# Optimization experiments

Measured on AMD Instinct MI355X. Metric: run time of the kernel, lower is better.

The kernel has to match this reference:

```python
import jax, jax.numpy as jnp
import numpy as np

ALPHA = 0.2        # LeakyReLU negative slope
MASK_VAL = -9e15   # matches torch zero_vec constant
B, N, F, H, D = 32, 1024, 64, 3, 16  # batch, nodes, in_features, heads, head_dim


def setup_inputs() -> dict:
    key = jax.random.key(0)
    k1, k2, k3 = jax.random.split(key, 3)
    h = jax.random.normal(k1, (B, N, F), dtype=jnp.float32)
    adj = jnp.ones((N, N), dtype=jnp.float32)  # fully-connected graph ('full')
    W = jax.random.normal(k2, (H, F, D), dtype=jnp.float32) * 0.15  # ~xavier gain 1.414
    a = jax.random.normal(k3, (H, 2 * D, 1), dtype=jnp.float32) * 0.25
    return {"h": h, "adj": adj, "W": W, "a": a}


def reference(h, adj, W, a):
    # Multi-head GAT, vectorized over heads (original loops over heads).
    d = W.shape[-1]
    Wh = jnp.einsum('bnf,hfd->bhnd', h, W)              # (B,H,N,D)
    a1 = a[:, :d, 0]                                    # (H,D) -> applies to source node i
    a2 = a[:, d:, 0]                                    # (H,D) -> applies to target node j
    s1 = jnp.einsum('bhnd,hd->bhn', Wh, a1)             # (B,H,N)
    s2 = jnp.einsum('bhnd,hd->bhn', Wh, a2)             # (B,H,N)
    # e[b,h,i,j] = LeakyReLU(a1.Wh_i + a2.Wh_j) -- equivalent to the repeat/concat trick
    e = jax.nn.leaky_relu(s1[..., :, None] + s2[..., None, :], ALPHA)  # (B,H,N,N)
    e = jnp.where(adj > 0, e, MASK_VAL)
    attn = jax.nn.softmax(e, axis=-1)                   # softmax over neighbors j
    out = jnp.einsum('bhij,bhjd->bhid', attn, Wh)       # (B,H,N,D)
    # concat heads along feature dim: (B,N,H*D)
    Bn, Nn = h.shape[0], h.shape[1]
    return out.transpose(0, 2, 1, 3).reshape(Bn, Nn, -1)
```

## Files before the change

kernel.cpp:

```cpp
#include <hip/hip_runtime.h>
#include <math.h>

constexpr int Bc = 32, Nn = 1024, Fc = 64, Hc = 3, Dc = 16;
constexpr float ALPHAc = 0.2f;
constexpr float L2E    = 1.44269504088896340736f;

__device__ __forceinline__ unsigned enc_f32(float x) {
    unsigned b = __builtin_bit_cast(unsigned, x);
    return (b & 0x80000000u) ? ~b : (b | 0x80000000u);
}
__device__ __forceinline__ float dec_f32(unsigned e) {
    unsigned b = (e & 0x80000000u) ? (e ^ 0x80000000u) : ~e;
    return __builtin_bit_cast(float, b);
}

template <int CTRL, int RMASK, bool BC>
__device__ __forceinline__ float dpp_acc(float x) {
    int s = __builtin_amdgcn_update_dpp(0, __builtin_bit_cast(int, x),
                                        CTRL, RMASK, 0xF, BC);
    return x + __builtin_bit_cast(float, s);
}
__device__ __forceinline__ float wave_incl_scan(float x) {
    x = dpp_acc<0x111, 0xF, true >(x);
    x = dpp_acc<0x112, 0xF, true >(x);
    x = dpp_acc<0x114, 0xF, true >(x);
    x = dpp_acc<0x118, 0xF, true >(x);
    x = dpp_acc<0x142, 0xa, false>(x);
    x = dpp_acc<0x143, 0xc, false>(x);
    return x;
}

__device__ __forceinline__ unsigned lane_xor(unsigned x, int s) {
    if (s == 1)
        return (unsigned)__builtin_amdgcn_update_dpp(0, (int)x, 0xB1, 0xF, 0xF, true);
    if (s == 2)
        return (unsigned)__builtin_amdgcn_update_dpp(0, (int)x, 0x4E, 0xF, 0xF, true);
    return (unsigned)__shfl_xor((int)x, s, 64);
}

__global__ __launch_bounds__(1024, 1) void gat_one(
    const float* __restrict__ hbuf, const float* __restrict__ W,
    const float* __restrict__ a, const float* __restrict__ adj,
    unsigned* __restrict__ rowful, float* Whf, float* __restrict__ out)
{
    __shared__ __align__(16) float    PS[1025 * 35];
    __shared__ __align__(16) unsigned skA[Nn], skB[Nn];
    __shared__ __align__(16) float    s2o[Nn];
    __shared__ float    wtot[16][34];
    __shared__ unsigned wmiss[16];

    int bh = blockIdx.x;
    int hh = bh % Hc, b = bh / Hc;
    int t  = threadIdx.x;
    int wv = t >> 6, lane = t & 63;

    int row0 = bh * 11;
    unsigned miss = 0;
#pragma unroll
    for (int rr = 0; rr < 11; ++rr) {
        int row = row0 + rr;
        if (row < Nn) {
            float av = adj[(size_t)row * Nn + t];
            miss |= (av > 0.f) ? 0u : (1u << rr);
        }
    }
#pragma unroll
    for (int off = 1; off < 64; off <<= 1)
        miss |= (unsigned)__shfl_xor((int)miss, off, 64);
    if (lane == 0) wmiss[wv] = miss;
    __syncthreads();
    if (t < 11) {
        int row = row0 + t;
        if (row < Nn) {
            unsigned m = 0;
#pragma unroll
            for (int w2 = 0; w2 < 16; ++w2) m |= wmiss[w2];
            unsigned full = ((m >> t) & 1u) ^ 1u;
            unsigned val  = 0x5AFE0000u | ((unsigned)row << 1) | full;
            __hip_atomic_store(&rowful[row], val, __ATOMIC_RELAXED,
                               __HIP_MEMORY_SCOPE_AGENT);
        }
    }

    const float4* h4 = (const float4*)(hbuf + ((size_t)b * Nn + t) * Fc);
    const float*  Wp = W + (size_t)hh * Fc * Dc;

    float acc[Dc];
#pragma unroll
    for (int d = 0; d < Dc; ++d) acc[d] = 0.f;

#pragma unroll
    for (int q = 0; q < Fc / 4; ++q) {
        float4 hv = h4[q];
#pragma unroll
        for (int c = 0; c < 4; ++c) {
            float hv1 = (c == 0) ? hv.x : (c == 1) ? hv.y : (c == 2) ? hv.z : hv.w;
            const float4* wrp = (const float4*)(Wp + (4 * q + c) * Dc);
#pragma unroll
            for (int u = 0; u < 4; ++u) {
                float4 wq = wrp[u];
                acc[4*u+0] = fmaf(hv1, wq.x, acc[4*u+0]);
                acc[4*u+1] = fmaf(hv1, wq.y, acc[4*u+1]);
                acc[4*u+2] = fmaf(hv1, wq.z, acc[4*u+2]);
                acc[4*u+3] = fmaf(hv1, wq.w, acc[4*u+3]);
            }
        }
    }

    float4* wf = (float4*)(Whf + ((size_t)bh * Nn + t) * Dc);
#pragma unroll
    for (int u = 0; u < 4; ++u)
        wf[u] = make_float4(acc[4*u+0], acc[4*u+1], acc[4*u+2], acc[4*u+3]);

    const float* ap = a + (size_t)hh * 2 * Dc;
    float s1v = 0.f, s2v = 0.f;
#pragma unroll
    for (int d = 0; d < Dc; ++d) {
        s1v = fmaf(acc[d], ap[d],      s1v);
        s2v = fmaf(acc[d], ap[Dc + d], s2v);
    }
    s2o[t] = s2v;

    unsigned key = (enc_f32(s2v) & ~1023u) | (unsigned)t;

#pragma unroll
    for (int k = 2; k <= 64; k <<= 1) {
#pragma unroll
        for (int s = k >> 1; s >= 1; s >>= 1) {
            unsigned other = lane_xor(key, s);
            bool dirUp = ((t & k) == 0);
            bool lower = ((lane & s) == 0);
            unsigned mn = key < other ? key : other;
            unsigned mx = key < other ? other : key;
            key = (lower == dirUp) ? mn : mx;
        }
    }
    unsigned* bufs[2] = {skA, skB};
    int pb = 0;
#pragma unroll
    for (int k = 128; k <= 1024; k <<= 1) {
#pragma unroll
        for (int s = k >> 1; s >= 64; s >>= 1) {
            bufs[pb][t] = key;
            __syncthreads();
            unsigned other = bufs[pb][t ^ s];
            bool dirUp = ((t & k) == 0);
            bool lower = ((t & s) == 0);
            unsigned mn = key < other ? key : other;
            unsigned mx = key < other ? other : key;
            key = (lower == dirUp) ? mn : mx;
            pb ^= 1;
        }
#pragma unroll
        for (int s = 32; s >= 1; s >>= 1) {
            unsigned other = lane_xor(key, s);
            bool dirUp = ((t & k) == 0);
            bool lower = ((lane & s) == 0);
            unsigned mn = key < other ? key : other;
            unsigned mx = key < other ? other : key;
            key = (lower == dirUp) ? mn : mx;
        }
    }
    unsigned* sorted = bufs[pb];
    sorted[t] = key;

    int   j  = key & 1023u;
    float sv = dec_f32((key & ~1023u) | 512u);
    float Bv = __builtin_amdgcn_exp2f(sv * L2E);
    float Dv = __builtin_amdgcn_exp2f(sv * (ALPHAc * L2E));
    const float4* wr = (const float4*)(Whf + ((size_t)bh * Nn + j) * Dc);
    float4 w0 = wr[0], w1 = wr[1], w2 = wr[2], w3 = wr[3];
    float wh[16] = {w0.x,w0.y,w0.z,w0.w, w1.x,w1.y,w1.z,w1.w,
                    w2.x,w2.y,w2.z,w2.w, w3.x,w3.y,w3.z,w3.w};

    float v[34];
#pragma unroll
    for (int d = 0; d < 16; ++d) {
        v[d]      = Bv * wh[d];
        v[16 + d] = Dv * wh[d];
    }
    v[32] = Bv; v[33] = Dv;

#pragma unroll
    for (int c = 0; c < 34; ++c) {
        float inc = wave_incl_scan(v[c]);
        if (lane == 63) wtot[wv][c] = inc;
        v[c] = inc - v[c];
    }
    __syncthreads();

    if (t < 544) {
        int c = t >> 4, w = t & 15;
        float own = wtot[w][c];
        float x = own;
#pragma unroll
        for (int off = 1; off < 16; off <<= 1) {
            float o = __shfl_up(x, off, 16);
            if ((lane & 15) >= off) x += o;
        }
        wtot[w][c] = x - own;
        if (w == 15) PS[(size_t)1024 * 35 + c] = x;
    }
    __syncthreads();

    float* myrow = PS + (size_t)t * 35;
#pragma unroll
    for (int c = 0; c < 34; ++c)
        myrow[c] = v[c] + wtot[wv][c];
    __syncthreads();

    int i = t;
    float R  = __builtin_amdgcn_exp2f(-0.8f * L2E * s1v);
    float* op = out + ((size_t)b * Nn + i) * (Hc * Dc) + hh * Dc;

    unsigned expv = 0x5AFE0000u | ((unsigned)i << 1) | 1u;
    unsigned fv;
    do {
        fv = __hip_atomic_load(&rowful[i], __ATOMIC_RELAXED,
                               __HIP_MEMORY_SCOPE_AGENT);
    } while ((fv | 1u) != expv);

    if (fv & 1u) {
        unsigned qk = (enc_f32(-s1v) & ~1023u) | 1023u;
        int p = 0;
#pragma unroll
        for (int step = 512; step >= 1; step >>= 1)
            if (sorted[p + step - 1] <= qk) p += step;

        const float* Pp = PS + (size_t)p * 35;
        const float* Tp = PS + (size_t)1024 * 35;
        float den = (Tp[32] - Pp[32]) + R * Pp[33];
        float inv = 1.0f / den;
#pragma unroll
        for (int u = 0; u < 4; ++u) {
            float o0 = ((Tp[4*u+0] - Pp[4*u+0]) + R * Pp[16 + 4*u+0]) * inv;
            float o1 = ((Tp[4*u+1] - Pp[4*u+1]) + R * Pp[16 + 4*u+1]) * inv;
            float o2 = ((Tp[4*u+2] - Pp[4*u+2]) + R * Pp[16 + 4*u+2]) * inv;
            float o3 = ((Tp[4*u+3] - Pp[4*u+3]) + R * Pp[16 + 4*u+3]) * inv;
            ((float4*)op)[u] = make_float4(o0, o1, o2, o3);
        }
    } else {
        float num[16];
#pragma unroll
        for (int d = 0; d < 16; ++d) num[d] = 0.f;
        float den = 0.f;
        for (int q = 0; q < Nn; ++q) {
            float aq = adj[(size_t)i * Nn + q];
            if (aq > 0.f) {
                float sq = s2o[q];
                float Bq = __builtin_amdgcn_exp2f(sq * L2E);
                float Dq = __builtin_amdgcn_exp2f(sq * (ALPHAc * L2E));
                float w_ = fmaxf(Bq, R * Dq);
                den += w_;
                const float* wq = Whf + ((size_t)bh * Nn + q) * Dc;
#pragma unroll
                for (int d = 0; d < 16; ++d)
                    num[d] = fmaf(w_, wq[d], num[d]);
            }
        }
        float inv = 1.0f / den;
#pragma unroll
        for (int d = 0; d < 16; ++d) op[d] = num[d] * inv;
    }
}

extern "C" void kernel_launch(void* const* d_in, const int* in_sizes, int n_in,
                              void* d_out, int out_size, void* d_ws, size_t ws_size,
                              hipStream_t stream)
{
    const float* hbuf = (const float*)d_in[0];
    const float* adj  = (const float*)d_in[1];
    const float* W    = (const float*)d_in[2];
    const float* a    = (const float*)d_in[3];
    float* out = (float*)d_out;

    float* Whf       = (float*)d_ws;
    unsigned* rowful = (unsigned*)(Whf + (size_t)Bc * Hc * Nn * Dc);

    gat_one<<<dim3(Bc * Hc), dim3(1024), 0, stream>>>(
        hbuf, W, a, adj, rowful, Whf, out);
}
```

Baseline: 36.07 us.

## Stage Wh in LDS for sorted gather and overlap adjacency loads with projection

Wh rows are written into shared memory (the PS buffer, padded stride 20 with a rotated float4 layout to spread banks) so the post-sort gather by sorted index reads LDS instead of re-reading global Whf written moments earlier. The adjacency loads are issued up front into registers and their mask reduction is deferred until after the projection, overlapping that memory latency with compute. The risks are reuse of PS before its later use, which needs the existing syncthreads for correctness, and extra register pressure from holding eleven adjacency values.

```diff
diff --git a/kernel.cpp b/kernel.cpp
--- a/kernel.cpp
+++ b/kernel.cpp
@@ -55,14 +55,66 @@
     int wv = t >> 6, lane = t & 63;
 
     int row0 = bh * 11;
-    unsigned miss = 0;
+    float adjv[11];
 #pragma unroll
     for (int rr = 0; rr < 11; ++rr) {
         int row = row0 + rr;
-        if (row < Nn) {
-            float av = adj[(size_t)row * Nn + t];
-            miss |= (av > 0.f) ? 0u : (1u << rr);
-        }
+        int rc  = row < Nn ? row : Nn - 1;
+        adjv[rr] = adj[(size_t)rc * Nn + t];
+    }
+
+    const float4* h4 = (const float4*)(hbuf + ((size_t)b * Nn + t) * Fc);
+    const float*  Wp = W + (size_t)hh * Fc * Dc;
+
+    float acc[Dc];
+#pragma unroll
+    for (int d = 0; d < Dc; ++d) acc[d] = 0.f;
+
+#pragma unroll
+    for (int q = 0; q < Fc / 4; ++q) {
+        float4 hv = h4[q];
+#pragma unroll
+        for (int c = 0; c < 4; ++c) {
+            float hv1 = (c == 0) ? hv.x : (c == 1) ? hv.y : (c == 2) ? hv.z : hv.w;
+            const float4* wrp = (const float4*)(Wp + (4 * q + c) * Dc);
+#pragma unroll
+            for (int u = 0; u < 4; ++u) {
+                float4 wq = wrp[u];
+                acc[4*u+0] = fmaf(hv1, wq.x, acc[4*u+0]);
+                acc[4*u+1] = fmaf(hv1, wq.y, acc[4*u+1]);
+                acc[4*u+2] = fmaf(hv1, wq.z, acc[4*u+2]);
+                acc[4*u+3] = fmaf(hv1, wq.w, acc[4*u+3]);
+            }
+        }
+    }
+
+    float* WhL = PS;
+#pragma unroll
+    for (int u = 0; u < 4; ++u) {
+        int col = (u + (t >> 3)) & 3;
+        *(float4*)&WhL[t * 20 + col * 4] =
+            make_float4(acc[4*u+0], acc[4*u+1], acc[4*u+2], acc[4*u+3]);
+    }
+    float4* wf = (float4*)(Whf + ((size_t)bh * Nn + t) * Dc);
+#pragma unroll
+    for (int u = 0; u < 4; ++u)
+        wf[u] = make_float4(acc[4*u+0], acc[4*u+1], acc[4*u+2], acc[4*u+3]);
+
+    const float* ap = a + (size_t)hh * 2 * Dc;
+    float s1v = 0.f, s2v = 0.f;
+#pragma unroll
+    for (int d = 0; d < Dc; ++d) {
+        s1v = fmaf(acc[d], ap[d],      s1v);
+        s2v = fmaf(acc[d], ap[Dc + d], s2v);
+    }
+    s2o[t] = s2v;
+
+    unsigned miss = 0;
+#pragma unroll
+    for (int rr = 0; rr < 11; ++rr) {
+        int row = row0 + rr;
+        if (row < Nn)
+            miss |= (adjv[rr] > 0.f) ? 0u : (1u << rr);
     }
 #pragma unroll
     for (int off = 1; off < 64; off <<= 1)
@@ -81,45 +133,6 @@
                                __HIP_MEMORY_SCOPE_AGENT);
         }
     }
-
-    const float4* h4 = (const float4*)(hbuf + ((size_t)b * Nn + t) * Fc);
-    const float*  Wp = W + (size_t)hh * Fc * Dc;
-
-    float acc[Dc];
-#pragma unroll
-    for (int d = 0; d < Dc; ++d) acc[d] = 0.f;
-
-#pragma unroll
-    for (int q = 0; q < Fc / 4; ++q) {
-        float4 hv = h4[q];
-#pragma unroll
-        for (int c = 0; c < 4; ++c) {
-            float hv1 = (c == 0) ? hv.x : (c == 1) ? hv.y : (c == 2) ? hv.z : hv.w;
-            const float4* wrp = (const float4*)(Wp + (4 * q + c) * Dc);
-#pragma unroll
-            for (int u = 0; u < 4; ++u) {
-                float4 wq = wrp[u];
-                acc[4*u+0] = fmaf(hv1, wq.x, acc[4*u+0]);
-                acc[4*u+1] = fmaf(hv1, wq.y, acc[4*u+1]);
-                acc[4*u+2] = fmaf(hv1, wq.z, acc[4*u+2]);
-                acc[4*u+3] = fmaf(hv1, wq.w, acc[4*u+3]);
-            }
-        }
-    }
-
-    float4* wf = (float4*)(Whf + ((size_t)bh * Nn + t) * Dc);
-#pragma unroll
-    for (int u = 0; u < 4; ++u)
-        wf[u] = make_float4(acc[4*u+0], acc[4*u+1], acc[4*u+2], acc[4*u+3]);
-
-    const float* ap = a + (size_t)hh * 2 * Dc;
-    float s1v = 0.f, s2v = 0.f;
-#pragma unroll
-    for (int d = 0; d < Dc; ++d) {
-        s1v = fmaf(acc[d], ap[d],      s1v);
-        s2v = fmaf(acc[d], ap[Dc + d], s2v);
-    }
-    s2o[t] = s2v;
 
     unsigned key = (enc_f32(s2v) & ~1023u) | (unsigned)t;
 
@@ -168,10 +181,17 @@
     float sv = dec_f32((key & ~1023u) | 512u);
     float Bv = __builtin_amdgcn_exp2f(sv * L2E);
     float Dv = __builtin_amdgcn_exp2f(sv * (ALPHAc * L2E));
-    const float4* wr = (const float4*)(Whf + ((size_t)bh * Nn + j) * Dc);
-    float4 w0 = wr[0], w1 = wr[1], w2 = wr[2], w3 = wr[3];
-    float wh[16] = {w0.x,w0.y,w0.z,w0.w, w1.x,w1.y,w1.z,w1.w,
-                    w2.x,w2.y,w2.z,w2.w, w3.x,w3.y,w3.z,w3.w};
+
+    float4 g[4];
+#pragma unroll
+    for (int c = 0; c < 4; ++c)
+        g[c] = *(const float4*)&WhL[j * 20 + c * 4];
+    float wh[16];
+#pragma unroll
+    for (int u = 0; u < 4; ++u) {
+        float4 wq = g[(u + (j >> 3)) & 3];
+        wh[4*u+0] = wq.x; wh[4*u+1] = wq.y; wh[4*u+2] = wq.z; wh[4*u+3] = wq.w;
+    }
 
     float v[34];
 #pragma unroll
```

Result: slower. 37.87 us (+5.0%).
